# Kernel optimization log

Measured on AMD Instinct MI355X. Metric: run time of the kernel, lower is better.

## Reference

```python
import jax, jax.numpy as jnp
import numpy as np

N_NODES = 20000
N_EDGES = 640000
NUM_COUNTS = 64
NUM_FEATS = 128


def setup_inputs() -> dict:
    key = jax.random.key(0)
    k1, k2, k3, k4, k5 = jax.random.split(key, 5)
    cnt = jax.random.uniform(k1, (N_EDGES, NUM_COUNTS), dtype=jnp.float32)
    embedding = jax.random.normal(k2, (N_NODES, NUM_FEATS), dtype=jnp.float32)
    importance = jax.random.normal(k3, (NUM_COUNTS, NUM_FEATS), dtype=jnp.float32)
    src = jax.random.randint(k4, (N_EDGES,), 0, N_NODES, dtype=jnp.int32)
    # ensure every node has >=1 incoming edge so the normalization divide is well-defined
    dst = jax.random.permutation(k5, jnp.arange(N_EDGES, dtype=jnp.int32) % N_NODES)
    return {"cnt": cnt, "embedding": embedding, "importance": importance, "src": src, "dst": dst}


def reference(cnt, embedding, importance, src, dst):
    # weight = softmax over the num_counts axis (dim=0)
    weight = jax.nn.softmax(importance, axis=0)            # [C, F]
    edge_score = cnt @ weight                               # [E, F] dense GEMM
    msgs = embedding[src] * edge_score                      # [E, F] u_mul_e
    new_embedding = jax.ops.segment_sum(msgs, dst, num_segments=N_NODES)      # [N, F]
    node_score = jax.ops.segment_sum(edge_score, dst, num_segments=N_NODES)   # [N, F]
    return new_embedding / node_score
```

## Files before the change

### kernel.cpp

```cpp
#include <hip/hip_runtime.h>
#include <hip/hip_bf16.h>
#include <stdint.h>

#define NN 20000
#define NE 640000
#define NC 64
#define NF 128
#define CAP 32
#define ESTRIDE 132
#define NPW 5
#define WPB 4

typedef __attribute__((ext_vector_type(8))) short short8;
typedef __attribute__((ext_vector_type(8))) __bf16 bf16x8;
typedef __attribute__((ext_vector_type(2))) __bf16 bf16x2;
typedef __attribute__((ext_vector_type(4))) float floatx4;
typedef __attribute__((ext_vector_type(4))) unsigned int uintx4;

static __device__ __forceinline__ unsigned short f2bf(float f) {
  union { float f; unsigned int i; } v; v.f = f;
  unsigned int x = v.i;
  x += 0x7fffu + ((x >> 16) & 1u);
  return (unsigned short)(x >> 16);
}

static __device__ __forceinline__ unsigned int pk2(float a, float b) {
#if __has_builtin(__builtin_amdgcn_cvt_pk_bf16_f32)
  bf16x2 r = __builtin_amdgcn_cvt_pk_bf16_f32(a, b);
  return __builtin_bit_cast(unsigned int, r);
#else
  return (unsigned int)f2bf(a) | ((unsigned int)f2bf(b) << 16);
#endif
}

static __device__ __forceinline__ short8 cvt8(floatx4 lo, floatx4 hi) {
  uintx4 u;
  u.x = pk2(lo[0], lo[1]); u.y = pk2(lo[2], lo[3]);
  u.z = pk2(hi[0], hi[1]); u.w = pk2(hi[2], hi[3]);
  return __builtin_bit_cast(short8, u);
}

static __device__ __forceinline__ float frcp(float x) {
#if __has_builtin(__builtin_amdgcn_rcpf)
  return __builtin_amdgcn_rcpf(x);
#else
  return 1.0f / x;
#endif
}

__global__ void softpack_kernel(const float* __restrict__ imp,
                                unsigned short* __restrict__ wpack) {
  __shared__ float w_s[NC][NF];
  int f = threadIdx.x;
  float v[NC];
  float mx = -1e30f;
#pragma unroll
  for (int c = 0; c < NC; ++c) { v[c] = imp[c * NF + f]; mx = fmaxf(mx, v[c]); }
  float s = 0.f;
#pragma unroll
  for (int c = 0; c < NC; ++c) { v[c] = __expf(v[c] - mx); s += v[c]; }
  float inv = 1.0f / s;
#pragma unroll
  for (int c = 0; c < NC; ++c) w_s[c][f] = v[c] * inv;
  __syncthreads();
#pragma unroll
  for (int idx = 0; idx < 8192; idx += 128) {
    int i2 = idx + f;
    int j  = i2 & 7;
    int l  = (i2 >> 3) & 63;
    int ks = (i2 >> 9) & 1;
    int nt = i2 >> 10;
    int k = ks * 32 + (l >> 4) * 8 + j;
    int n = nt * 16 + (l & 15);
    wpack[i2] = f2bf(w_s[k][n]);
  }
}

__global__ void bin_kernel(const int* __restrict__ dst,
                           int* __restrict__ counts,
                           int* __restrict__ elist,
                           int cstride) {
  int e = blockIdx.x * 256 + threadIdx.x;
  if (e < NE) {
    int n = dst[e];
    int slot = atomicAdd(&counts[(size_t)n * cstride], 1);
    if (slot < CAP) elist[n * CAP + slot] = e;
  }
}

__global__ __launch_bounds__(256) void node_kernel(
    const float* __restrict__ cnt,
    const float* __restrict__ emb,
    const int* __restrict__ srcp,
    const int* __restrict__ elist,
    const unsigned short* __restrict__ wpack,
    float* __restrict__ out)
{
  __shared__ float es_s[WPB][16 * ESTRIDE];
  __shared__ int eids_s[WPB][2][CAP];
  __shared__ int srcs_s[WPB][2][CAP];

  const int tid = threadIdx.x;
  const int wid = tid >> 6;
  const int lane = tid & 63;
  const int m = lane & 15;
  const int q = lane >> 4;
  const int base = (blockIdx.x * WPB + wid) * NPW;
  float* es = es_s[wid];

  short8 wf[8][2];
#pragma unroll
  for (int nt = 0; nt < 8; ++nt)
#pragma unroll
    for (int ks = 0; ks < 2; ++ks)
      wf[nt][ks] = *(const short8*)(wpack + ((nt * 2 + ks) * 64 + lane) * 8);

  if (lane < CAP) {
    int e0 = elist[(size_t)base * CAP + lane];
    eids_s[wid][0][lane] = e0;
    srcs_s[wid][0][lane] = srcp[e0];
  }

  for (int i = 0; i < NPW; ++i) {
    const int buf = i & 1;
    const int node = base + i;
    const bool do_pre = (i + 1 < NPW) && (lane < CAP);

    int pe = 0, ps = 0;
    if (do_pre) pe = elist[(size_t)(node + 1) * CAP + lane];

    asm volatile("s_waitcnt lgkmcnt(0)" ::: "memory");

    int eid0 = eids_s[wid][buf][m];
    int eid1 = eids_s[wid][buf][16 + m];

    float ea[8], sa[8];
#pragma unroll
    for (int j = 0; j < 8; ++j) { ea[j] = 0.f; sa[j] = 0.f; }

#pragma unroll
    for (int h = 0; h < 2; ++h) {
      const float* crow = cnt + (size_t)(h ? eid1 : eid0) * NC + q * 8;
      floatx4 c0 = *(const floatx4*)(crow);
      floatx4 c1 = *(const floatx4*)(crow + 4);
      floatx4 c2 = *(const floatx4*)(crow + 32);
      floatx4 c3 = *(const floatx4*)(crow + 36);
      short8 a0 = cvt8(c0, c1);
      short8 a1 = cvt8(c2, c3);

      floatx4 acc[8];
#pragma unroll
      for (int nt = 0; nt < 8; ++nt)
#pragma unroll
        for (int r = 0; r < 4; ++r) acc[nt][r] = 0.f;
#pragma unroll
      for (int nt = 0; nt < 8; ++nt) {
        acc[nt] = __builtin_amdgcn_mfma_f32_16x16x32_bf16(
            __builtin_bit_cast(bf16x8, a0), __builtin_bit_cast(bf16x8, wf[nt][0]),
            acc[nt], 0, 0, 0);
        acc[nt] = __builtin_amdgcn_mfma_f32_16x16x32_bf16(
            __builtin_bit_cast(bf16x8, a1), __builtin_bit_cast(bf16x8, wf[nt][1]),
            acc[nt], 0, 0, 0);
      }

#pragma unroll
      for (int nt = 0; nt < 8; ++nt)
#pragma unroll
        for (int r = 0; r < 4; ++r)
          es[(q * 4 + r) * ESTRIDE + nt * 16 + m] = acc[nt][r];

      if (h == 0 && do_pre) ps = srcp[pe];

      asm volatile("s_waitcnt lgkmcnt(0)" ::: "memory");

#pragma unroll
      for (int t = 0; t < 4; ++t) {
        int el = q + 4 * t;
        floatx4 p0 = *(const floatx4*)&es[el * ESTRIDE + m * 8];
        floatx4 p1 = *(const floatx4*)&es[el * ESTRIDE + m * 8 + 4];
        int s = srcs_s[wid][buf][h * 16 + el];
        const float* erow = emb + (size_t)s * NF + m * 8;
        floatx4 e0 = *(const floatx4*)erow;
        floatx4 e1 = *(const floatx4*)(erow + 4);
#pragma unroll
        for (int j = 0; j < 4; ++j) {
          ea[j]     = fmaf(p0[j], e0[j], ea[j]);
          ea[j + 4] = fmaf(p1[j], e1[j], ea[j + 4]);
          sa[j]     += p0[j];
          sa[j + 4] += p1[j];
        }
      }
      asm volatile("" ::: "memory");
    }

    if (do_pre) { eids_s[wid][buf ^ 1][lane] = pe; srcs_s[wid][buf ^ 1][lane] = ps; }

#pragma unroll
    for (int j = 0; j < 8; ++j) {
      ea[j] += __shfl_xor(ea[j], 16, 64);
      ea[j] += __shfl_xor(ea[j], 32, 64);
      sa[j] += __shfl_xor(sa[j], 16, 64);
      sa[j] += __shfl_xor(sa[j], 32, 64);
    }

    if (lane < 16) {
      floatx4 o0, o1;
#pragma unroll
      for (int p = 0; p < 4; ++p) {
        o0[p] = ea[p] * frcp(sa[p]);
        o1[p] = ea[p + 4] * frcp(sa[p + 4]);
      }
      float* op = out + (size_t)node * NF + lane * 8;
      *(floatx4*)op = o0;
      *(floatx4*)(op + 4) = o1;
    }
  }
}

extern "C" void kernel_launch(void* const* d_in, const int* in_sizes, int n_in,
                              void* d_out, int out_size, void* d_ws, size_t ws_size,
                              hipStream_t stream) {
  const float* cnt = (const float*)d_in[0];
  const float* emb = (const float*)d_in[1];
  const float* imp = (const float*)d_in[2];
  const int* src = (const int*)d_in[3];
  const int* dst = (const int*)d_in[4];
  float* out = (float*)d_out;

  char* ws = (char*)d_ws;
  unsigned short* wpack = (unsigned short*)(ws);

  const size_t need_padded = 16384 + (size_t)NN * 32 + (size_t)NN * CAP * 4;
  int cstride;
  int* counts;
  int* elist;
  if (ws_size >= need_padded) {
    cstride = 8;
    counts = (int*)(ws + 16384);
    elist  = (int*)(ws + 16384 + (size_t)NN * 32);
  } else {
    cstride = 1;
    counts = (int*)(ws + 16384);
    elist  = (int*)(ws + 98304);
  }

  hipMemsetAsync(counts, 0, (size_t)NN * cstride * sizeof(int), stream);
  softpack_kernel<<<1, NF, 0, stream>>>(imp, wpack);
  bin_kernel<<<(NE + 255) / 256, 256, 0, stream>>>(dst, counts, elist, cstride);
  node_kernel<<<NN / (WPB * NPW), 256, 0, stream>>>(cnt, emb, src, elist, wpack, out);
}
```

Measured before the change: 301.1 us.

## Software-pipeline cnt row loads one node ahead and keep edge ids in registers

Replaces the LDS double buffers for edge and source ids with register-held values that are distributed across lanes with wave shuffles, and prefetches the edge list two nodes ahead. The cnt rows for the next node are now issued to global memory before the current node's gather and reduce phase, so their latency overlaps with work. Both MFMA halves are computed from operands already held in registers. This trades higher VGPR pressure (eight extra floatx4 prefetch registers) for hiding the dependent cnt-load latency, and the added registers could lower occupancy.

```diff
diff --git a/kernel.cpp b/kernel.cpp
--- a/kernel.cpp
+++ b/kernel.cpp
@@ -97,8 +97,6 @@
     float* __restrict__ out)
 {
   __shared__ float es_s[WPB][16 * ESTRIDE];
-  __shared__ int eids_s[WPB][2][CAP];
-  __shared__ int srcs_s[WPB][2][CAP];
 
   const int tid = threadIdx.x;
   const int wid = tid >> 6;
@@ -115,85 +113,127 @@
     for (int ks = 0; ks < 2; ++ks)
       wf[nt][ks] = *(const short8*)(wpack + ((nt * 2 + ks) * 64 + lane) * 8);
 
+  int e_cur = 0, e_nxt = 0, s_cur = 0;
   if (lane < CAP) {
-    int e0 = elist[(size_t)base * CAP + lane];
-    eids_s[wid][0][lane] = e0;
-    srcs_s[wid][0][lane] = srcp[e0];
-  }
+    e_cur = elist[(size_t)base * CAP + lane];
+    int n1 = base + 1 < NN ? base + 1 : NN - 1;
+    e_nxt = elist[(size_t)n1 * CAP + lane];
+    s_cur = srcp[e_cur];
+  }
+  int eid0 = __shfl(e_cur, m, 64);
+  int eid1 = __shfl(e_cur, 16 + m, 64);
+  const float* r0 = cnt + (size_t)eid0 * NC + q * 8;
+  const float* r1 = cnt + (size_t)eid1 * NC + q * 8;
+  floatx4 cc0 = *(const floatx4*)(r0);      floatx4 cc1 = *(const floatx4*)(r0 + 4);
+  floatx4 cc2 = *(const floatx4*)(r0 + 32); floatx4 cc3 = *(const floatx4*)(r0 + 36);
+  floatx4 cc4 = *(const floatx4*)(r1);      floatx4 cc5 = *(const floatx4*)(r1 + 4);
+  floatx4 cc6 = *(const floatx4*)(r1 + 32); floatx4 cc7 = *(const floatx4*)(r1 + 36);
 
   for (int i = 0; i < NPW; ++i) {
-    const int buf = i & 1;
     const int node = base + i;
-    const bool do_pre = (i + 1 < NPW) && (lane < CAP);
-
-    int pe = 0, ps = 0;
-    if (do_pre) pe = elist[(size_t)(node + 1) * CAP + lane];
+
+    int e_n2 = 0;
+    if (i + 2 < NPW && lane < CAP)
+      e_n2 = elist[(size_t)(node + 2) * CAP + lane];
+
+    short8 a00 = cvt8(cc0, cc1), a01 = cvt8(cc2, cc3);
+    short8 a10 = cvt8(cc4, cc5), a11 = cvt8(cc6, cc7);
+
+    floatx4 acc[8];
+#pragma unroll
+    for (int nt = 0; nt < 8; ++nt)
+#pragma unroll
+      for (int r = 0; r < 4; ++r) acc[nt][r] = 0.f;
+#pragma unroll
+    for (int nt = 0; nt < 8; ++nt) {
+      acc[nt] = __builtin_amdgcn_mfma_f32_16x16x32_bf16(
+          __builtin_bit_cast(bf16x8, a00), __builtin_bit_cast(bf16x8, wf[nt][0]),
+          acc[nt], 0, 0, 0);
+      acc[nt] = __builtin_amdgcn_mfma_f32_16x16x32_bf16(
+          __builtin_bit_cast(bf16x8, a01), __builtin_bit_cast(bf16x8, wf[nt][1]),
+          acc[nt], 0, 0, 0);
+    }
+#pragma unroll
+    for (int nt = 0; nt < 8; ++nt)
+#pragma unroll
+      for (int r = 0; r < 4; ++r)
+        es[(q * 4 + r) * ESTRIDE + nt * 16 + m] = acc[nt][r];
+
+    int s_nxt = 0;
+    if (i + 1 < NPW) {
+      int eid0n = __shfl(e_nxt, m, 64);
+      int eid1n = __shfl(e_nxt, 16 + m, 64);
+      const float* n0 = cnt + (size_t)eid0n * NC + q * 8;
+      const float* n1 = cnt + (size_t)eid1n * NC + q * 8;
+      cc0 = *(const floatx4*)(n0);      cc1 = *(const floatx4*)(n0 + 4);
+      cc2 = *(const floatx4*)(n0 + 32); cc3 = *(const floatx4*)(n0 + 36);
+      cc4 = *(const floatx4*)(n1);      cc5 = *(const floatx4*)(n1 + 4);
+      cc6 = *(const floatx4*)(n1 + 32); cc7 = *(const floatx4*)(n1 + 36);
+      if (lane < CAP) s_nxt = srcp[e_nxt];
+    }
+
+    float ea[8], sa[8];
+#pragma unroll
+    for (int j = 0; j < 8; ++j) { ea[j] = 0.f; sa[j] = 0.f; }
 
     asm volatile("s_waitcnt lgkmcnt(0)" ::: "memory");
-
-    int eid0 = eids_s[wid][buf][m];
-    int eid1 = eids_s[wid][buf][16 + m];
-
-    float ea[8], sa[8];
-#pragma unroll
-    for (int j = 0; j < 8; ++j) { ea[j] = 0.f; sa[j] = 0.f; }
-
-#pragma unroll
-    for (int h = 0; h < 2; ++h) {
-      const float* crow = cnt + (size_t)(h ? eid1 : eid0) * NC + q * 8;
-      floatx4 c0 = *(const floatx4*)(crow);
-      floatx4 c1 = *(const floatx4*)(crow + 4);
-      floatx4 c2 = *(const floatx4*)(crow + 32);
-      floatx4 c3 = *(const floatx4*)(crow + 36);
-      short8 a0 = cvt8(c0, c1);
-      short8 a1 = cvt8(c2, c3);
-
-      floatx4 acc[8];
-#pragma unroll
-      for (int nt = 0; nt < 8; ++nt)
-#pragma unroll
-        for (int r = 0; r < 4; ++r) acc[nt][r] = 0.f;
-#pragma unroll
-      for (int nt = 0; nt < 8; ++nt) {
-        acc[nt] = __builtin_amdgcn_mfma_f32_16x16x32_bf16(
-            __builtin_bit_cast(bf16x8, a0), __builtin_bit_cast(bf16x8, wf[nt][0]),
-            acc[nt], 0, 0, 0);
-        acc[nt] = __builtin_amdgcn_mfma_f32_16x16x32_bf16(
-            __builtin_bit_cast(bf16x8, a1), __builtin_bit_cast(bf16x8, wf[nt][1]),
-            acc[nt], 0, 0, 0);
+#pragma unroll
+    for (int t = 0; t < 4; ++t) {
+      int el = q + 4 * t;
+      floatx4 p0 = *(const floatx4*)&es[el * ESTRIDE + m * 8];
+      floatx4 p1 = *(const floatx4*)&es[el * ESTRIDE + m * 8 + 4];
+      int s = __shfl(s_cur, el, 64);
+      const float* erow = emb + (size_t)s * NF + m * 8;
+      floatx4 e0 = *(const floatx4*)erow;
+      floatx4 e1 = *(const floatx4*)(erow + 4);
+#pragma unroll
+      for (int j = 0; j < 4; ++j) {
+        ea[j]     = fmaf(p0[j], e0[j], ea[j]);
+        ea[j + 4] = fmaf(p1[j], e1[j], ea[j + 4]);
+        sa[j]     += p0[j];
+        sa[j + 4] += p1[j];
       }
-
-#pragma unroll
-      for (int nt = 0; nt < 8; ++nt)
-#pragma unroll
-        for (int r = 0; r < 4; ++r)
-          es[(q * 4 + r) * ESTRIDE + nt * 16 + m] = acc[nt][r];
-
-      if (h == 0 && do_pre) ps = srcp[pe];
-
-      asm volatile("s_waitcnt lgkmcnt(0)" ::: "memory");
-
-#pragma unroll
-      for (int t = 0; t < 4; ++t) {
-        int el = q + 4 * t;
-        floatx4 p0 = *(const floatx4*)&es[el * ESTRIDE + m * 8];
-        floatx4 p1 = *(const floatx4*)&es[el * ESTRIDE + m * 8 + 4];
-        int s = srcs_s[wid][buf][h * 16 + el];
-        const float* erow = emb + (size_t)s * NF + m * 8;
-        floatx4 e0 = *(const floatx4*)erow;
-        floatx4 e1 = *(const floatx4*)(erow + 4);
-#pragma unroll
-        for (int j = 0; j < 4; ++j) {
-          ea[j]     = fmaf(p0[j], e0[j], ea[j]);
-          ea[j + 4] = fmaf(p1[j], e1[j], ea[j + 4]);
-          sa[j]     += p0[j];
-          sa[j + 4] += p1[j];
-        }
+    }
+    asm volatile("" ::: "memory");
+
+#pragma unroll
+    for (int nt = 0; nt < 8; ++nt)
+#pragma unroll
+      for (int r = 0; r < 4; ++r) acc[nt][r] = 0.f;
+#pragma unroll
+    for (int nt = 0; nt < 8; ++nt) {
+      acc[nt] = __builtin_amdgcn_mfma_f32_16x16x32_bf16(
+          __builtin_bit_cast(bf16x8, a10), __builtin_bit_cast(bf16x8, wf[nt][0]),
+          acc[nt], 0, 0, 0);
+      acc[nt] = __builtin_amdgcn_mfma_f32_16x16x32_bf16(
+          __builtin_bit_cast(bf16x8, a11), __builtin_bit_cast(bf16x8, wf[nt][1]),
+          acc[nt], 0, 0, 0);
+    }
+#pragma unroll
+    for (int nt = 0; nt < 8; ++nt)
+#pragma unroll
+      for (int r = 0; r < 4; ++r)
+        es[(q * 4 + r) * ESTRIDE + nt * 16 + m] = acc[nt][r];
+
+    asm volatile("s_waitcnt lgkmcnt(0)" ::: "memory");
+#pragma unroll
+    for (int t = 0; t < 4; ++t) {
+      int el = q + 4 * t;
+      floatx4 p0 = *(const floatx4*)&es[el * ESTRIDE + m * 8];
+      floatx4 p1 = *(const floatx4*)&es[el * ESTRIDE + m * 8 + 4];
+      int s = __shfl(s_cur, 16 + el, 64);
+      const float* erow = emb + (size_t)s * NF + m * 8;
+      floatx4 e0 = *(const floatx4*)erow;
+      floatx4 e1 = *(const floatx4*)(erow + 4);
+#pragma unroll
+      for (int j = 0; j < 4; ++j) {
+        ea[j]     = fmaf(p0[j], e0[j], ea[j]);
+        ea[j + 4] = fmaf(p1[j], e1[j], ea[j + 4]);
+        sa[j]     += p0[j];
+        sa[j + 4] += p1[j];
       }
-      asm volatile("" ::: "memory");
-    }
-
-    if (do_pre) { eids_s[wid][buf ^ 1][lane] = pe; srcs_s[wid][buf ^ 1][lane] = ps; }
+    }
+    asm volatile("" ::: "memory");
 
 #pragma unroll
     for (int j = 0; j < 8; ++j) {
@@ -214,6 +254,10 @@
       *(floatx4*)op = o0;
       *(floatx4*)(op + 4) = o1;
     }
+
+    e_cur = e_nxt;
+    e_nxt = e_n2;
+    s_cur = s_nxt;
   }
 }
 
```

After: 306.3 us. About the same (+1.7%).

## Software-pipeline cnt and embedding loads across halves and nodes, use register shuffles

Applied to the files above, without the earlier changes.

Restructures the per-node loop so the next half's (or next node's) cnt rows are loaded before the current half's consume phase, and embedding rows are issued around the MFMA block to overlap latency. Edge ids and source ids now live in registers and are distributed with wave shuffles instead of LDS double-buffers, with a two-deep prefetch of elist. This raises register pressure and leaves a dead shuffle block, but aims to hide global memory latency behind MFMA and LDS work.

```diff
diff --git a/kernel.cpp b/kernel.cpp
--- a/kernel.cpp
+++ b/kernel.cpp
@@ -88,6 +88,46 @@
   }
 }
 
+#define CONSUME(EL, E0, E1)                                                   \
+  {                                                                           \
+    floatx4 p0 = *(const floatx4*)&es[(EL) * ESTRIDE + m * 8];                \
+    floatx4 p1 = *(const floatx4*)&es[(EL) * ESTRIDE + m * 8 + 4];            \
+    _Pragma("unroll")                                                         \
+    for (int j = 0; j < 4; ++j) {                                             \
+      ea[j]     = fmaf(p0[j], (E0)[j], ea[j]);                                \
+      ea[j + 4] = fmaf(p1[j], (E1)[j], ea[j + 4]);                            \
+      sa[j]     += p0[j];                                                     \
+      sa[j + 4] += p1[j];                                                     \
+    }                                                                         \
+  }
+
+#define LOADE(E0, E1, S)                                                      \
+  {                                                                           \
+    const float* _p = emb + (size_t)(S) * NF + m * 8;                         \
+    E0 = *(const floatx4*)_p;                                                 \
+    E1 = *(const floatx4*)(_p + 4);                                           \
+  }
+
+#define MFMA16(A0, A1)                                                        \
+  _Pragma("unroll")                                                           \
+  for (int nt = 0; nt < 8; ++nt) {                                            \
+    _Pragma("unroll")                                                         \
+    for (int r = 0; r < 4; ++r) acc[nt][r] = 0.f;                             \
+    acc[nt] = __builtin_amdgcn_mfma_f32_16x16x32_bf16(                        \
+        __builtin_bit_cast(bf16x8, A0), __builtin_bit_cast(bf16x8, wf[nt][0]),\
+        acc[nt], 0, 0, 0);                                                    \
+    acc[nt] = __builtin_amdgcn_mfma_f32_16x16x32_bf16(                        \
+        __builtin_bit_cast(bf16x8, A1), __builtin_bit_cast(bf16x8, wf[nt][1]),\
+        acc[nt], 0, 0, 0);                                                    \
+  }
+
+#define STORE_ACC                                                             \
+  _Pragma("unroll")                                                           \
+  for (int nt = 0; nt < 8; ++nt)                                              \
+    _Pragma("unroll")                                                         \
+    for (int r = 0; r < 4; ++r)                                               \
+      es[(q * 4 + r) * ESTRIDE + nt * 16 + m] = acc[nt][r];
+
 __global__ __launch_bounds__(256) void node_kernel(
     const float* __restrict__ cnt,
     const float* __restrict__ emb,
@@ -97,8 +137,6 @@
     float* __restrict__ out)
 {
   __shared__ float es_s[WPB][16 * ESTRIDE];
-  __shared__ int eids_s[WPB][2][CAP];
-  __shared__ int srcs_s[WPB][2][CAP];
 
   const int tid = threadIdx.x;
   const int wid = tid >> 6;
@@ -115,85 +153,88 @@
     for (int ks = 0; ks < 2; ++ks)
       wf[nt][ks] = *(const short8*)(wpack + ((nt * 2 + ks) * 64 + lane) * 8);
 
+  int e_cur = 0, e_nxt = 0, s_cur = 0;
   if (lane < CAP) {
-    int e0 = elist[(size_t)base * CAP + lane];
-    eids_s[wid][0][lane] = e0;
-    srcs_s[wid][0][lane] = srcp[e0];
+    e_cur = elist[(size_t)base * CAP + lane];
+    s_cur = srcp[e_cur];
+    e_nxt = elist[(size_t)(base + 1) * CAP + lane];
+  }
+  {
+    int eid0 = __shfl(e_cur, m, 64);
+    const float* rr = cnt + (size_t)eid0 * NC + q * 8;
+  }
+  floatx4 c0, c1, c2, c3;
+  {
+    int eid0 = __shfl(e_cur, m, 64);
+    const float* rr = cnt + (size_t)eid0 * NC + q * 8;
+    c0 = *(const floatx4*)rr;        c1 = *(const floatx4*)(rr + 4);
+    c2 = *(const floatx4*)(rr + 32); c3 = *(const floatx4*)(rr + 36);
   }
 
   for (int i = 0; i < NPW; ++i) {
-    const int buf = i & 1;
     const int node = base + i;
-    const bool do_pre = (i + 1 < NPW) && (lane < CAP);
-
-    int pe = 0, ps = 0;
-    if (do_pre) pe = elist[(size_t)(node + 1) * CAP + lane];
-
-    asm volatile("s_waitcnt lgkmcnt(0)" ::: "memory");
-
-    int eid0 = eids_s[wid][buf][m];
-    int eid1 = eids_s[wid][buf][16 + m];
+
+    int s0[4], s1[4];
+#pragma unroll
+    for (int t = 0; t < 4; ++t) {
+      s0[t] = __shfl(s_cur, q + 4 * t, 64);
+      s1[t] = __shfl(s_cur, 16 + q + 4 * t, 64);
+    }
+    int e_n2 = 0, s_nxt = 0;
+    if (i + 2 < NPW && lane < CAP)
+      e_n2 = elist[(size_t)(node + 2) * CAP + lane];
 
     float ea[8], sa[8];
 #pragma unroll
     for (int j = 0; j < 8; ++j) { ea[j] = 0.f; sa[j] = 0.f; }
 
-#pragma unroll
-    for (int h = 0; h < 2; ++h) {
-      const float* crow = cnt + (size_t)(h ? eid1 : eid0) * NC + q * 8;
-      floatx4 c0 = *(const floatx4*)(crow);
-      floatx4 c1 = *(const floatx4*)(crow + 4);
-      floatx4 c2 = *(const floatx4*)(crow + 32);
-      floatx4 c3 = *(const floatx4*)(crow + 36);
-      short8 a0 = cvt8(c0, c1);
-      short8 a1 = cvt8(c2, c3);
-
-      floatx4 acc[8];
-#pragma unroll
-      for (int nt = 0; nt < 8; ++nt)
-#pragma unroll
-        for (int r = 0; r < 4; ++r) acc[nt][r] = 0.f;
-#pragma unroll
-      for (int nt = 0; nt < 8; ++nt) {
-        acc[nt] = __builtin_amdgcn_mfma_f32_16x16x32_bf16(
-            __builtin_bit_cast(bf16x8, a0), __builtin_bit_cast(bf16x8, wf[nt][0]),
-            acc[nt], 0, 0, 0);
-        acc[nt] = __builtin_amdgcn_mfma_f32_16x16x32_bf16(
-            __builtin_bit_cast(bf16x8, a1), __builtin_bit_cast(bf16x8, wf[nt][1]),
-            acc[nt], 0, 0, 0);
+    floatx4 acc[8];
+    floatx4 Ea0, Ea1, Eb0, Eb1, Ec0, Ec1, Ed0, Ed1;
+
+    {
+      short8 a0 = cvt8(c0, c1), a1 = cvt8(c2, c3);
+      LOADE(Ea0, Ea1, s0[0]);
+      LOADE(Eb0, Eb1, s0[1]);
+      MFMA16(a0, a1);
+      STORE_ACC;
+      LOADE(Ec0, Ec1, s0[2]);
+      LOADE(Ed0, Ed1, s0[3]);
+      {
+        int eid1 = __shfl(e_cur, 16 + m, 64);
+        const float* rr = cnt + (size_t)eid1 * NC + q * 8;
+        c0 = *(const floatx4*)rr;        c1 = *(const floatx4*)(rr + 4);
+        c2 = *(const floatx4*)(rr + 32); c3 = *(const floatx4*)(rr + 36);
       }
-
-#pragma unroll
-      for (int nt = 0; nt < 8; ++nt)
-#pragma unroll
-        for (int r = 0; r < 4; ++r)
-          es[(q * 4 + r) * ESTRIDE + nt * 16 + m] = acc[nt][r];
-
-      if (h == 0 && do_pre) ps = srcp[pe];
-
+      if (i + 1 < NPW && lane < CAP) s_nxt = srcp[e_nxt];
       asm volatile("s_waitcnt lgkmcnt(0)" ::: "memory");
-
-#pragma unroll
-      for (int t = 0; t < 4; ++t) {
-        int el = q + 4 * t;
-        floatx4 p0 = *(const floatx4*)&es[el * ESTRIDE + m * 8];
-        floatx4 p1 = *(const floatx4*)&es[el * ESTRIDE + m * 8 + 4];
-        int s = srcs_s[wid][buf][h * 16 + el];
-        const float* erow = emb + (size_t)s * NF + m * 8;
-        floatx4 e0 = *(const floatx4*)erow;
-        floatx4 e1 = *(const floatx4*)(erow + 4);
-#pragma unroll
-        for (int j = 0; j < 4; ++j) {
-          ea[j]     = fmaf(p0[j], e0[j], ea[j]);
-          ea[j + 4] = fmaf(p1[j], e1[j], ea[j + 4]);
-          sa[j]     += p0[j];
-          sa[j + 4] += p1[j];
-        }
+      CONSUME(q,      Ea0, Ea1);
+      CONSUME(q + 4,  Eb0, Eb1);
+      CONSUME(q + 8,  Ec0, Ec1);
+      CONSUME(q + 12, Ed0, Ed1);
+      asm volatile("" ::: "memory");
+    }
+
+    {
+      short8 a0 = cvt8(c0, c1), a1 = cvt8(c2, c3);
+      LOADE(Ea0, Ea1, s1[0]);
+      LOADE(Eb0, Eb1, s1[1]);
+      MFMA16(a0, a1);
+      STORE_ACC;
+      LOADE(Ec0, Ec1, s1[2]);
+      LOADE(Ed0, Ed1, s1[3]);
+      if (i + 1 < NPW) {
+        int eid0n = __shfl(e_nxt, m, 64);
+        const float* rr = cnt + (size_t)eid0n * NC + q * 8;
+        c0 = *(const floatx4*)rr;        c1 = *(const floatx4*)(rr + 4);
+        c2 = *(const floatx4*)(rr + 32); c3 = *(const floatx4*)(rr + 36);
       }
+      asm volatile("s_waitcnt lgkmcnt(0)" ::: "memory");
+      CONSUME(q,      Ea0, Ea1);
+      CONSUME(q + 4,  Eb0, Eb1);
+      CONSUME(q + 8,  Ec0, Ec1);
+      CONSUME(q + 12, Ed0, Ed1);
       asm volatile("" ::: "memory");
     }
-
-    if (do_pre) { eids_s[wid][buf ^ 1][lane] = pe; srcs_s[wid][buf ^ 1][lane] = ps; }
 
 #pragma unroll
     for (int j = 0; j < 8; ++j) {
@@ -214,6 +255,10 @@
       *(floatx4*)op = o0;
       *(floatx4*)(op + 4) = o1;
     }
+
+    e_cur = e_nxt;
+    e_nxt = e_n2;
+    s_cur = s_nxt;
   }
 }
 
```

Result: slower. 308.8 us (+2.6%).
